# Kernel tuning notes

Hardware: AMD Instinct MI355X
Metric: run time of the kernel (lower is better)

Reference implementation:

```python
import jax, jax.numpy as jnp
import numpy as np

MODES = 16
IN_CH = 64
OUT_CH = 64
SCALE = 1.0 / (IN_CH * OUT_CH)


def setup_inputs() -> dict:
    key = jax.random.key(0)
    k1, k2, k3 = jax.random.split(key, 3)
    v = jax.random.normal(k1, (32, IN_CH, 8192), dtype=jnp.float32)
    # torch.rand on cfloat -> uniform [0,1) real and imag parts, then scaled
    w_real = jax.random.uniform(k2, (MODES, OUT_CH, IN_CH), dtype=jnp.float32) * SCALE
    w_imag = jax.random.uniform(k3, (MODES, OUT_CH, IN_CH), dtype=jnp.float32) * SCALE
    return {"v": v, "w_real": w_real, "w_imag": w_imag}


def reference(v, w_real, w_imag):
    # v: [B, Cin, N]; weights: [modes, Cout, Cin] complex
    W = w_real + 1j * w_imag
    vf = jnp.fft.rfft(v)                      # [B, Cin, Nf], complex64
    nf = vf.shape[-1]
    # 'koi,bki->bko' with bki = vf[:,:, :modes] transposed -> equivalently:
    lv = jnp.einsum('koi,bik->bok', W, vf[:, :, :MODES])  # [B, Cout, modes]
    lv_full = jnp.pad(lv, ((0, 0), (0, 0), (0, nf - MODES)))  # zero high modes
    return jnp.fft.irfft(lv_full, n=v.shape[-1])  # [B, Cout, N] real
```

## Files before the change

### kernel.cpp

```cpp
#include <hip/hip_runtime.h>
#include <math.h>

#define NN 8192
#define NMODES 16
#define NB 32
#define NCH 64
#define NROWS (NB * NCH)
#define TPB 256
#define JIT 8

#define K8 0.70710678118654752440f

struct KCTab { float c[16][4]; float s[16][4]; };
constexpr KCTab make_kc() {
  KCTab r{};
  for (int k = 0; k < 16; ++k)
    for (int c = 0; c < 4; ++c) {
      double th = 6.283185307179586476925287 * (double)(k * c) / 8192.0;
      double x2 = th * th;
      r.c[k][c] = (float)(1.0 - x2 / 2.0 + x2 * x2 / 24.0 - x2 * x2 * x2 / 720.0);
      r.s[k][c] = (float)(th - th * x2 / 6.0 + th * x2 * x2 / 120.0 - th * x2 * x2 * x2 / 5040.0);
    }
  return r;
}
constexpr KCTab KCT = make_kc();

__device__ __forceinline__ void rotacc8(int m, float x, float& br, float& bi) {
  switch (m) {
    case 0: br += x; break;
    case 1: br = fmaf(x,  K8, br); bi = fmaf(x, -K8, bi); break;
    case 2: bi -= x; break;
    case 3: br = fmaf(x, -K8, br); bi = fmaf(x, -K8, bi); break;
    case 4: br -= x; break;
    case 5: br = fmaf(x, -K8, br); bi = fmaf(x,  K8, bi); break;
    case 6: bi += x; break;
    default: br = fmaf(x,  K8, br); bi = fmaf(x,  K8, bi); break;
  }
}

__device__ __forceinline__ float synth8(int m, float dr, float di, float acc) {
  switch (m) {
    case 0: return acc + dr;
    case 1: return fmaf(K8, dr - di, acc);
    case 2: return acc - di;
    case 3: return fmaf(-K8, dr + di, acc);
    case 4: return acc - dr;
    case 5: return fmaf(K8, di - dr, acc);
    case 6: return acc + di;
    default: return fmaf(K8, dr + di, acc);
  }
}

__global__ __launch_bounds__(TPB) void fwd_dft_kernel(
    const float* __restrict__ v, float* __restrict__ vfpart) {
  const int row = blockIdx.x;
  const int t = threadIdx.x;
  const float4* __restrict__ vr4 = (const float4*)(v + (size_t)row * NN);

  float br[4][8], bi[4][8];
#pragma unroll
  for (int c = 0; c < 4; ++c)
#pragma unroll
    for (int m = 0; m < 8; ++m) { br[c][m] = 0.f; bi[c][m] = 0.f; }

#pragma unroll
  for (int j = 0; j < JIT; ++j) {
    const float4 x = vr4[t + TPB * j];
#pragma unroll
    for (int m = 0; m < 8; ++m) {
      const int e = (m * j) & 7;
      rotacc8(e, x.x, br[0][m], bi[0][m]);
      rotacc8(e, x.y, br[1][m], bi[1][m]);
      rotacc8(e, x.z, br[2][m], bi[2][m]);
      rotacc8(e, x.w, br[3][m], bi[3][m]);
    }
  }

  double phi = (double)t * (6.283185307179586476925287 / 2048.0);
  double spd, cpd;
  sincos(phi, &spd, &cpd);
  const float c1 = (float)cpd, s1 = (float)spd;

  float pr[NMODES], pi[NMODES];
  float ck = 1.f, sk = 0.f;
#pragma unroll
  for (int k = 0; k < NMODES; ++k) {
    const int m = k & 7;
    float ar = br[0][m], ai = bi[0][m];
#pragma unroll
    for (int c = 1; c < 4; ++c) {
      ar = fmaf(br[c][m], KCT.c[k][c], fmaf(bi[c][m],  KCT.s[k][c], ar));
      ai = fmaf(bi[c][m], KCT.c[k][c], fmaf(br[c][m], -KCT.s[k][c], ai));
    }
    pr[k] = ar * ck + ai * sk;
    pi[k] = ai * ck - ar * sk;
    const float cn = ck * c1 - sk * s1;
    const float sn = sk * c1 + ck * s1;
    ck = cn; sk = sn;
  }

  const int lane = t & 63, wave = t >> 6;

  float u16[16];
  {
    const bool hi = (lane & 16) != 0;
#pragma unroll
    for (int i = 0; i < 16; ++i) {
      const float send = hi ? pr[i] : pi[i];
      const float recv = __shfl_xor(send, 16);
      u16[i] = (hi ? pi[i] : pr[i]) + recv;
    }
  }
  float u8[8];
  {
    const bool hi = (lane & 8) != 0;
#pragma unroll
    for (int i = 0; i < 8; ++i) {
      const float send = hi ? u16[i] : u16[i + 8];
      const float recv = __shfl_xor(send, 8);
      u8[i] = (hi ? u16[i + 8] : u16[i]) + recv;
    }
  }
  float u4[4];
  {
    const bool hi = (lane & 4) != 0;
#pragma unroll
    for (int i = 0; i < 4; ++i) {
      const float send = hi ? u8[i] : u8[i + 4];
      const float recv = __shfl_xor(send, 4);
      u4[i] = (hi ? u8[i + 4] : u8[i]) + recv;
    }
  }
  float u2[2];
  {
    const bool hi = (lane & 2) != 0;
#pragma unroll
    for (int i = 0; i < 2; ++i) {
      const float send = hi ? u4[i] : u4[i + 2];
      const float recv = __shfl_xor(send, 2);
      u2[i] = (hi ? u4[i + 2] : u4[i]) + recv;
    }
  }
  float u1;
  {
    const bool hi = (lane & 1) != 0;
    const float send = hi ? u2[0] : u2[1];
    const float recv = __shfl_xor(send, 1);
    u1 = (hi ? u2[1] : u2[0]) + recv;
  }
  const float total = u1 + __shfl_xor(u1, 32);

  if (lane < 32) {
    vfpart[((size_t)row * 4 + wave) * 32 + lane] = total;
  }
}

__global__ __launch_bounds__(TPB) void mix_inv_kernel(
    const float* __restrict__ vfpart, const float* __restrict__ wre,
    const float* __restrict__ wim, float* __restrict__ out) {
  const int bid = blockIdx.x;
  const int b = bid >> 6, o = bid & 63;
  const int t = threadIdx.x;

  __shared__ float red[16][33];
  __shared__ float lvs[32];

  {
    const int k = t & 15, g = t >> 4;
    float lr = 0.f, li = 0.f;
#pragma unroll
    for (int ii = 0; ii < 4; ++ii) {
      const int i = g * 4 + ii;
      const float* __restrict__ p = vfpart + (size_t)(b * NCH + i) * 128;
      float vr = 0.f, vi = 0.f;
#pragma unroll
      for (int w = 0; w < 4; ++w) {
        vr += p[w * 32 + k];
        vi += p[w * 32 + 16 + k];
      }
      const float wr = wre[((size_t)k * NCH + o) * NCH + i];
      const float wi = wim[((size_t)k * NCH + o) * NCH + i];
      lr = fmaf(wr, vr, fmaf(-wi, vi, lr));
      li = fmaf(wr, vi, fmaf( wi, vr, li));
    }
    red[g][k]      = lr;
    red[g][16 + k] = li;
  }
  __syncthreads();
  if (t < 32) {
    float s = 0.f;
#pragma unroll
    for (int g = 0; g < 16; ++g) s += red[g][t];
    const float gk = ((t & 15) == 0) ? (1.0f / (float)NN) : (2.0f / (float)NN);
    lvs[t] = s * gk;
  }
  __syncthreads();

  double phi = (double)t * (6.283185307179586476925287 / 2048.0);
  double spd, cpd;
  sincos(phi, &spd, &cpd);
  const float c1 = (float)cpd, s1 = (float)spd;

  float Er[4][8], Ei[4][8];
  {
    float Dr[4][NMODES], Di[4][NMODES];
    float ck = 1.f, sk = 0.f;
#pragma unroll
    for (int k = 0; k < NMODES; ++k) {
      const float Ar = lvs[k], Ai = lvs[16 + k];
      const float xr = Ar * ck - Ai * sk;
      const float xi = Ai * ck + Ar * sk;
      Dr[0][k] = xr; Di[0][k] = xi;
#pragma unroll
      for (int c = 1; c < 4; ++c) {
        Dr[c][k] = fmaf(xr, KCT.c[k][c], -xi * KCT.s[k][c]);
        Di[c][k] = fmaf(xi, KCT.c[k][c],  xr * KCT.s[k][c]);
      }
      const float cn = ck * c1 - sk * s1;
      const float sn = sk * c1 + ck * s1;
      ck = cn; sk = sn;
    }
#pragma unroll
    for (int c = 0; c < 4; ++c)
#pragma unroll
      for (int m = 0; m < 8; ++m) {
        Er[c][m] = Dr[c][m] + Dr[c][m + 8];
        Ei[c][m] = Di[c][m] + Di[c][m + 8];
      }
  }

  float4* __restrict__ out4 = (float4*)(out + (size_t)bid * NN);
#pragma unroll
  for (int j = 0; j < JIT; ++j) {
    float a0 = 0.f, a1 = 0.f, a2 = 0.f, a3 = 0.f;
#pragma unroll
    for (int m = 0; m < 8; ++m) {
      const int e = (m * j) & 7;
      a0 = synth8(e, Er[0][m], Ei[0][m], a0);
      a1 = synth8(e, Er[1][m], Ei[1][m], a1);
      a2 = synth8(e, Er[2][m], Ei[2][m], a2);
      a3 = synth8(e, Er[3][m], Ei[3][m], a3);
    }
    float4 r; r.x = a0; r.y = a1; r.z = a2; r.w = a3;
    out4[t + TPB * j] = r;
  }
}

extern "C" void kernel_launch(void* const* d_in, const int* in_sizes, int n_in,
                              void* d_out, int out_size, void* d_ws, size_t ws_size,
                              hipStream_t stream) {
  const float* v   = (const float*)d_in[0];
  const float* wre = (const float*)d_in[1];
  const float* wim = (const float*)d_in[2];
  float* out = (float*)d_out;

  float* vfpart = (float*)d_ws;

  fwd_dft_kernel<<<NROWS, TPB, 0, stream>>>(v, vfpart);
  mix_inv_kernel<<<NROWS, TPB, 0, stream>>>(vfpart, wre, wim, out);
}
```

Before: 34.89 us.

## Replace direct 8-point DFT accumulation with radix-2 butterflies and nontemporal I/O

The per-thread 8-point forward DFT, previously done as 64 rotate-accumulates per lane, is replaced by an explicit 8-point FFT butterfly that exploits real-input symmetry. The inverse synthesis uses an 8-point inverse butterfly with Hermitian folding. Both kernels switch to nontemporal vector loads and stores to keep streamed data from polluting cache. It also folds mode pairs into running sums in place to cut register pressure, and adds a dead, no-op tweak to a shuffle stage.

```diff
diff --git a/kernel.cpp b/kernel.cpp
--- a/kernel.cpp
+++ b/kernel.cpp
@@ -7,9 +7,10 @@
 #define NCH 64
 #define NROWS (NB * NCH)
 #define TPB 256
-#define JIT 8
 
 #define K8 0.70710678118654752440f
+
+typedef float f32x4 __attribute__((ext_vector_type(4)));
 
 struct KCTab { float c[16][4]; float s[16][4]; };
 constexpr KCTab make_kc() {
@@ -25,55 +26,33 @@
 }
 constexpr KCTab KCT = make_kc();
 
-__device__ __forceinline__ void rotacc8(int m, float x, float& br, float& bi) {
-  switch (m) {
-    case 0: br += x; break;
-    case 1: br = fmaf(x,  K8, br); bi = fmaf(x, -K8, bi); break;
-    case 2: bi -= x; break;
-    case 3: br = fmaf(x, -K8, br); bi = fmaf(x, -K8, bi); break;
-    case 4: br -= x; break;
-    case 5: br = fmaf(x, -K8, br); bi = fmaf(x,  K8, bi); break;
-    case 6: bi += x; break;
-    default: br = fmaf(x,  K8, br); bi = fmaf(x,  K8, bi); break;
-  }
-}
-
-__device__ __forceinline__ float synth8(int m, float dr, float di, float acc) {
-  switch (m) {
-    case 0: return acc + dr;
-    case 1: return fmaf(K8, dr - di, acc);
-    case 2: return acc - di;
-    case 3: return fmaf(-K8, dr + di, acc);
-    case 4: return acc - dr;
-    case 5: return fmaf(K8, di - dr, acc);
-    case 6: return acc + di;
-    default: return fmaf(K8, dr + di, acc);
-  }
-}
-
 __global__ __launch_bounds__(TPB) void fwd_dft_kernel(
     const float* __restrict__ v, float* __restrict__ vfpart) {
   const int row = blockIdx.x;
   const int t = threadIdx.x;
-  const float4* __restrict__ vr4 = (const float4*)(v + (size_t)row * NN);
-
-  float br[4][8], bi[4][8];
-#pragma unroll
-  for (int c = 0; c < 4; ++c)
-#pragma unroll
-    for (int m = 0; m < 8; ++m) { br[c][m] = 0.f; bi[c][m] = 0.f; }
-
-#pragma unroll
-  for (int j = 0; j < JIT; ++j) {
-    const float4 x = vr4[t + TPB * j];
-#pragma unroll
-    for (int m = 0; m < 8; ++m) {
-      const int e = (m * j) & 7;
-      rotacc8(e, x.x, br[0][m], bi[0][m]);
-      rotacc8(e, x.y, br[1][m], bi[1][m]);
-      rotacc8(e, x.z, br[2][m], bi[2][m]);
-      rotacc8(e, x.w, br[3][m], bi[3][m]);
-    }
+  const f32x4* __restrict__ vr4 = (const f32x4*)(v + (size_t)row * NN);
+
+  float x[4][8];
+#pragma unroll
+  for (int j = 0; j < 8; ++j) {
+    const f32x4 q = __builtin_nontemporal_load(vr4 + t + TPB * j);
+    x[0][j] = q.x; x[1][j] = q.y; x[2][j] = q.z; x[3][j] = q.w;
+  }
+
+  float X0[4], X4[4], X1r[4], X1i[4], X2r[4], X2i[4], X3r[4], X3i[4];
+#pragma unroll
+  for (int c = 0; c < 4; ++c) {
+    const float a  = x[c][0] + x[c][4], b = x[c][0] - x[c][4];
+    const float cc = x[c][2] + x[c][6], d = x[c][2] - x[c][6];
+    const float e  = x[c][1] + x[c][5], f = x[c][1] - x[c][5];
+    const float g  = x[c][3] + x[c][7], h = x[c][3] - x[c][7];
+    const float t1 = a + cc, t2 = e + g;
+    X0[c]  = t1 + t2;
+    X4[c]  = t1 - t2;
+    X2r[c] = a - cc;  X2i[c] = g - e;
+    const float u = K8 * (f - h), w = K8 * (f + h);
+    X1r[c] = b + u;   X1i[c] = -d - w;
+    X3r[c] = b - u;   X3i[c] = d - w;
   }
 
   double phi = (double)t * (6.283185307179586476925287 / 2048.0);
@@ -86,11 +65,25 @@
 #pragma unroll
   for (int k = 0; k < NMODES; ++k) {
     const int m = k & 7;
-    float ar = br[0][m], ai = bi[0][m];
-#pragma unroll
-    for (int c = 1; c < 4; ++c) {
-      ar = fmaf(br[c][m], KCT.c[k][c], fmaf(bi[c][m],  KCT.s[k][c], ar));
-      ai = fmaf(bi[c][m], KCT.c[k][c], fmaf(br[c][m], -KCT.s[k][c], ai));
+    float ar = 0.f, ai = 0.f;
+#pragma unroll
+    for (int c = 0; c < 4; ++c) {
+      float br, bi;
+      switch (m) {
+        case 0:  br = X0[c];  bi = 0.f;      break;
+        case 1:  br = X1r[c]; bi = X1i[c];   break;
+        case 2:  br = X2r[c]; bi = X2i[c];   break;
+        case 3:  br = X3r[c]; bi = X3i[c];   break;
+        case 4:  br = X4[c];  bi = 0.f;      break;
+        case 5:  br = X3r[c]; bi = -X3i[c];  break;
+        case 6:  br = X2r[c]; bi = -X2i[c];  break;
+        default: br = X1r[c]; bi = -X1i[c];  break;
+      }
+      if (c == 0) { ar = br; ai = bi; }
+      else {
+        ar = fmaf(br, KCT.c[k][c], fmaf(bi,  KCT.s[k][c], ar));
+        ai = fmaf(bi, KCT.c[k][c], fmaf(br, -KCT.s[k][c], ai));
+      }
     }
     pr[k] = ar * ck + ai * sk;
     pi[k] = ai * ck - ar * sk;
@@ -136,8 +129,10 @@
     const bool hi = (lane & 2) != 0;
 #pragma unroll
     for (int i = 0; i < 2; ++i) {
-      const float send = hi ? u4[i] : u4[i + 2];
-      const float recv = __shfl_xor(send, 2);
+      const float send = hi ? u2[i] * 0.f + (hi ? u4[i] : u4[i + 2]) : u4[i + 2];
+      (void)send;
+      const float s2 = hi ? u4[i] : u4[i + 2];
+      const float recv = __shfl_xor(s2, 2);
       u2[i] = (hi ? u4[i + 2] : u4[i]) + recv;
     }
   }
@@ -203,46 +198,55 @@
 
   float Er[4][8], Ei[4][8];
   {
-    float Dr[4][NMODES], Di[4][NMODES];
     float ck = 1.f, sk = 0.f;
 #pragma unroll
     for (int k = 0; k < NMODES; ++k) {
+      const int m = k & 7;
       const float Ar = lvs[k], Ai = lvs[16 + k];
       const float xr = Ar * ck - Ai * sk;
       const float xi = Ai * ck + Ar * sk;
-      Dr[0][k] = xr; Di[0][k] = xi;
+      if (k < 8) { Er[0][m] = xr; Ei[0][m] = xi; }
+      else       { Er[0][m] += xr; Ei[0][m] += xi; }
 #pragma unroll
       for (int c = 1; c < 4; ++c) {
-        Dr[c][k] = fmaf(xr, KCT.c[k][c], -xi * KCT.s[k][c]);
-        Di[c][k] = fmaf(xi, KCT.c[k][c],  xr * KCT.s[k][c]);
+        const float dr = fmaf(xr, KCT.c[k][c], -xi * KCT.s[k][c]);
+        const float di = fmaf(xi, KCT.c[k][c],  xr * KCT.s[k][c]);
+        if (k < 8) { Er[c][m] = dr; Ei[c][m] = di; }
+        else       { Er[c][m] += dr; Ei[c][m] += di; }
       }
       const float cn = ck * c1 - sk * s1;
       const float sn = sk * c1 + ck * s1;
       ck = cn; sk = sn;
     }
-#pragma unroll
-    for (int c = 0; c < 4; ++c)
-#pragma unroll
-      for (int m = 0; m < 8; ++m) {
-        Er[c][m] = Dr[c][m] + Dr[c][m + 8];
-        Ei[c][m] = Di[c][m] + Di[c][m + 8];
-      }
-  }
-
-  float4* __restrict__ out4 = (float4*)(out + (size_t)bid * NN);
-#pragma unroll
-  for (int j = 0; j < JIT; ++j) {
-    float a0 = 0.f, a1 = 0.f, a2 = 0.f, a3 = 0.f;
-#pragma unroll
-    for (int m = 0; m < 8; ++m) {
-      const int e = (m * j) & 7;
-      a0 = synth8(e, Er[0][m], Ei[0][m], a0);
-      a1 = synth8(e, Er[1][m], Ei[1][m], a1);
-      a2 = synth8(e, Er[2][m], Ei[2][m], a2);
-      a3 = synth8(e, Er[3][m], Ei[3][m], a3);
-    }
-    float4 r; r.x = a0; r.y = a1; r.z = a2; r.w = a3;
-    out4[t + TPB * j] = r;
+  }
+
+  float y[4][8];
+#pragma unroll
+  for (int c = 0; c < 4; ++c) {
+    const float P0 = Er[c][0], P4 = Er[c][4];
+    const float P1 = Er[c][1] + Er[c][7], Q1 = Ei[c][1] - Ei[c][7];
+    const float P2 = Er[c][2] + Er[c][6], Q2 = Ei[c][2] - Ei[c][6];
+    const float P3 = Er[c][3] + Er[c][5], Q3 = Ei[c][3] - Ei[c][5];
+    const float s04 = P0 + P4, d04 = P0 - P4;
+    const float e0 = s04 + P2, e2 = s04 - P2;
+    const float e1 = d04 - Q2, e3 = d04 + Q2;
+    const float alpha = P1 - P3, beta = Q1 + Q3;
+    const float O0 = P1 + P3;
+    const float O2 = Q3 - Q1;
+    const float O1 =  K8 * (alpha - beta);
+    const float O3 = -K8 * (alpha + beta);
+    y[c][0] = e0 + O0; y[c][4] = e0 - O0;
+    y[c][1] = e1 + O1; y[c][5] = e1 - O1;
+    y[c][2] = e2 + O2; y[c][6] = e2 - O2;
+    y[c][3] = e3 + O3; y[c][7] = e3 - O3;
+  }
+
+  f32x4* __restrict__ out4 = (f32x4*)(out + (size_t)bid * NN);
+#pragma unroll
+  for (int j = 0; j < 8; ++j) {
+    f32x4 r;
+    r.x = y[0][j]; r.y = y[1][j]; r.z = y[2][j]; r.w = y[3][j];
+    __builtin_nontemporal_store(r, out4 + t + TPB * j);
   }
 }
 
```

Result: slower. 41.53 us (+19.0%).
